# Kernel optimization log

Measured on AMD Instinct MI355X. Metric: run time of the kernel, lower is better.

The kernel has to match this reference:

```python
import jax, jax.numpy as jnp
import numpy as np
from jax import lax

K = 3  # AdaConv kernel_size inside conv_block


def conv2d(x, w, b, pad):
    # x: (B,C,H,W), w: (O,I,kh,kw) -> NCHW conv with symmetric padding
    y = lax.conv_general_dilated(x, w, (1, 1), [(pad, pad), (pad, pad)],
                                 dimension_numbers=('NCHW', 'OIHW', 'NCHW'))
    return y + b[None, :, None, None]


def unfold3(x):
    # nn.Unfold(kernel=3, pad=1): patches ordered channel-major then (kh,kw) row-major
    B, C, H, W = x.shape
    xp = jnp.pad(x, ((0, 0), (0, 0), (1, 1), (1, 1)))
    return jnp.stack([xp[:, :, i:i + H, j:j + W]
                      for i in range(K) for j in range(K)], axis=2)  # (B,C,9,H,W)


def adaconv(x, mask, aw_w, aw_b, mt_w, mt_b, c_w, c_b):
    # groups=1, groups_channels=out_ch in this configuration
    weight = conv2d(mask, aw_w, aw_b, pad=2)          # (B, 9, H, W)
    x = conv2d(x, c_w, c_b, pad=1)                    # (B, out_ch, H, W)
    p = unfold3(x)                                    # (B, out_ch, 9, H, W)
    out = jnp.einsum('bkhw,bckhw->bchw', weight, p)   # per-pixel adaptive conv
    mask2 = conv2d(mask, mt_w, mt_b, pad=2)
    return out, mask2


def lrelu(x):
    return jax.nn.leaky_relu(x, 0.01)


def setup_inputs() -> dict:
    key = jax.random.key(0)
    ks = jax.random.split(key, 20)
    B, Cin, Cout, Mi, Mo, H, W = 2, 64, 64, 64, 64, 256, 256
    s = 0.05
    d = {
        'x': jax.random.normal(ks[0], (B, Cin, H, W), jnp.float32),
        'mask': jax.random.normal(ks[1], (B, Mi, H, W), jnp.float32),
        # AdaConv 1 (in_ch->out_ch, mask_in->mask_out)
        'aw1_w': jax.random.normal(ks[2], (K * K, Mi, 2 * K - 1, 2 * K - 1), jnp.float32) * s,
        'aw1_b': jax.random.normal(ks[3], (K * K,), jnp.float32) * s,
        'mt1_w': jax.random.normal(ks[4], (Mo, Mi, 2 * K - 1, 2 * K - 1), jnp.float32) * s,
        'mt1_b': jax.random.normal(ks[5], (Mo,), jnp.float32) * s,
        'c1_w': jax.random.normal(ks[6], (Cout, Cin, K, K), jnp.float32) * s,
        'c1_b': jax.random.normal(ks[7], (Cout,), jnp.float32) * s,
        # AdaConv 2 (out_ch->out_ch, mask_out->mask_out)
        'aw2_w': jax.random.normal(ks[8], (K * K, Mo, 2 * K - 1, 2 * K - 1), jnp.float32) * s,
        'aw2_b': jax.random.normal(ks[9], (K * K,), jnp.float32) * s,
        'mt2_w': jax.random.normal(ks[10], (Mo, Mo, 2 * K - 1, 2 * K - 1), jnp.float32) * s,
        'mt2_b': jax.random.normal(ks[11], (Mo,), jnp.float32) * s,
        'c2_w': jax.random.normal(ks[12], (Cout, Cout, K, K), jnp.float32) * s,
        'c2_b': jax.random.normal(ks[13], (Cout,), jnp.float32) * s,
        # 1x1 residual conv
        'cr_w': jax.random.normal(ks[14], (Cout, Cin, 1, 1), jnp.float32) * s,
        'cr_b': jax.random.normal(ks[15], (Cout,), jnp.float32) * s,
    }
    return d


def reference(x, mask, aw1_w, aw1_b, mt1_w, mt1_b, c1_w, c1_b,
              aw2_w, aw2_b, mt2_w, mt2_b, c2_w, c2_b, cr_w, cr_b):
    res = conv2d(x, cr_w, cr_b, pad=0)
    x, mask = adaconv(x, mask, aw1_w, aw1_b, mt1_w, mt1_b, c1_w, c1_b)
    x, mask = lrelu(x), lrelu(mask)
    x, mask = adaconv(x, mask, aw2_w, aw2_b, mt2_w, mt2_b, c2_w, c2_b)
    x, mask = lrelu(x), lrelu(mask)
    return (x + res, mask)
```

## Files before the change

kernel.cpp:

```cpp
#include <hip/hip_runtime.h>

#define HWSZ 65536
#define CCH  64

typedef __bf16 bf16x8 __attribute__((ext_vector_type(8)));
typedef __bf16 bf16x4 __attribute__((ext_vector_type(4)));
typedef float  f32x4  __attribute__((ext_vector_type(4)));

__device__ inline void gload_lds16(const void* g, void* l) {
    __builtin_amdgcn_global_load_lds(
        (const __attribute__((address_space(1))) void*)g,
        (__attribute__((address_space(3))) void*)l, 16, 0, 0);
}

__global__ __launch_bounds__(256) void k_cvt(
    const float* __restrict__ src, __bf16* __restrict__ dst)
{
    int p  = blockIdx.x * 256 + threadIdx.x;
    int b  = p >> 16, hw = p & 65535;
    const float* sp = src + (((size_t)b * 64) << 16) + hw;
    __bf16* dp = dst + (size_t)p * 64;
    #pragma unroll
    for (int c8 = 0; c8 < 8; ++c8) {
        bf16x8 v8;
        #pragma unroll
        for (int j = 0; j < 8; ++j)
            v8[j] = (__bf16)sp[(size_t)(c8 * 8 + j) << 16];
        *(bf16x8*)(dp + c8 * 8) = v8;
    }
}

__global__ __launch_bounds__(256) void k_prep3(
    const float* __restrict__ src, __bf16* __restrict__ dst)
{
    int t = blockIdx.x * 256 + threadIdx.x;
    if (t >= 9 * 64 * 64) return;
    int j = t & 7;
    int u = (t >> 3) % 512;
    int k = t / 4096;
    int o = u >> 3;
    int s = (u & 7) ^ (o & 7);
    int i = s * 8 + j;
    dst[t] = (__bf16)src[((size_t)o * 64 + i) * 9 + k];
}

__global__ __launch_bounds__(256) void k_prepF(
    const float* __restrict__ mt, const float* __restrict__ aw,
    __bf16* __restrict__ dst)
{
    int t = blockIdx.x * 256 + threadIdx.x;
    if (t >= 25 * 96 * 64) return;
    int j = t & 7;
    int u = (t >> 3) % 768;
    int k = t / 6144;
    int r = u >> 3;
    int s = (u & 7) ^ (r & 7);
    int i = s * 8 + j;
    float v = 0.f;
    if (r < 64)      v = mt[((size_t)r * 64 + i) * 25 + k];
    else if (r < 73) v = aw[((size_t)(r - 64) * 64 + i) * 25 + k];
    dst[t] = (__bf16)v;
}

template<int KSZ, int MFT, int RELU, int EPI>
__global__ __launch_bounds__(256) void k_mconv(
    const __bf16* __restrict__ xh, const __bf16* __restrict__ wb,
    const float* __restrict__ bias, const float* __restrict__ bias2,
    float* __restrict__ outf, __bf16* __restrict__ outh,
    float* __restrict__ out2)
{
    constexpr int PAD   = KSZ / 2;
    constexpr int TW    = 16 + 2 * PAD;
    constexpr int NPIX  = TW * TW;
    constexpr int KK    = KSZ * KSZ;
    constexpr int SROWS = (MFT == 5) ? 96 : 64;
    constexpr int SLICE = SROWS * 128;
    constexpr int NISS  = SROWS / 32;

    __shared__ __align__(16) __bf16 lx[NPIX * 64];
    __shared__ __align__(16) __bf16 lw[2][SROWS * 64];
    __shared__ float lb[80];

    const int t    = threadIdx.x;
    const int w0   = blockIdx.x * 16, h0 = blockIdx.y * 16, b = blockIdx.z;
    const int wvv  = t >> 6;
    const int lane = t & 63;
    const int px   = lane & 15;
    const int g    = lane >> 4;

    auto STAGE = [&](int k, int buf) {
        const char* gs = (const char*)wb + (size_t)k * SLICE;
        char* lbase = (char*)lw[buf];
        #pragma unroll
        for (int r = 0; r < NISS; ++r) {
            int ub = (wvv * NISS + r) * 64;
            gload_lds16(gs + (ub + lane) * 16, lbase + ub * 16);
        }
    };

    STAGE(0, 0);
    STAGE(1, 1);

    if (t < 64) lb[t] = bias[t];
    if constexpr (MFT == 5) {
        if (t >= 64 && t < 80) lb[t] = (t - 64 < 9) ? bias2[t - 64] : 0.f;
    }

    bf16x8 zv;
    #pragma unroll
    for (int j = 0; j < 8; ++j) zv[j] = (__bf16)0.f;
    constexpr int PITER = (NPIX + 255) / 256;
    #pragma unroll
    for (int pi = 0; pi < PITER; ++pi) {
        int pix = pi * 256 + t;
        if (pix < NPIX) {
            int sy = pix / TW, sx = pix - sy * TW;
            int gy = h0 + sy - PAD, gx = w0 + sx - PAD;
            bool ok = (unsigned)gy < 256u && (unsigned)gx < 256u;
            const __bf16* src = xh + ((((size_t)b << 16) + gy * 256 + gx) << 6);
            int rowbase = pix << 7, sw = (pix & 7) << 4;
            #pragma unroll
            for (int c8 = 0; c8 < 8; ++c8) {
                bf16x8 v8 = ok ? *(const bf16x8*)(src + c8 * 8) : zv;
                *(bf16x8*)((char*)lx + rowbase + ((c8 << 4) ^ sw)) = v8;
            }
        }
    }
    __syncthreads();

    f32x4 acc[MFT][4];
    #pragma unroll
    for (int m = 0; m < MFT; ++m)
        #pragma unroll
        for (int nf = 0; nf < 4; ++nf)
            acc[m][nf] = (f32x4){0.f, 0.f, 0.f, 0.f};

    #pragma unroll
    for (int k = 0; k < KK; ++k) {
        const __bf16* lwb = lw[k & 1];
        const int dy = k / KSZ, dx = k - dy * KSZ;

        bf16x8 bfr[4][2];
        #pragma unroll
        for (int nf = 0; nf < 4; ++nf) {
            int pix = (wvv * 4 + nf + dy) * TW + (px + dx);
            int rowbase = pix << 7, sw = (pix & 7) << 4;
            #pragma unroll
            for (int ks = 0; ks < 2; ++ks)
                bfr[nf][ks] = *(const bf16x8*)((const char*)lx + rowbase + ((((ks * 4 + g) << 4)) ^ sw));
        }
        bf16x8 afr[MFT][2];
        #pragma unroll
        for (int m = 0; m < MFT; ++m) {
            int o = m * 16 + px;
            int rowbase = o << 7, sw = (o & 7) << 4;
            #pragma unroll
            for (int ks = 0; ks < 2; ++ks)
                afr[m][ks] = *(const bf16x8*)((const char*)lwb + rowbase + ((((ks * 4 + g) << 4)) ^ sw));
        }
        #pragma unroll
        for (int m = 0; m < MFT; ++m)
            #pragma unroll
            for (int nf = 0; nf < 4; ++nf)
                #pragma unroll
                for (int ks = 0; ks < 2; ++ks)
                    acc[m][nf] = __builtin_amdgcn_mfma_f32_16x16x32_bf16(
                        afr[m][ks], bfr[nf][ks], acc[m][nf], 0, 0, 0);

        if (k == KK - 1) break;

        asm volatile("s_waitcnt lgkmcnt(0)" ::: "memory");
        __builtin_amdgcn_sched_barrier(0);
        __builtin_amdgcn_s_barrier();
        bool issued = (k + 2 < KK);
        if (issued) {
            STAGE(k + 2, k & 1);
            if constexpr (NISS == 2) asm volatile("s_waitcnt vmcnt(2)" ::: "memory");
            else                     asm volatile("s_waitcnt vmcnt(3)" ::: "memory");
        } else {
            asm volatile("s_waitcnt vmcnt(0)" ::: "memory");
        }
        __builtin_amdgcn_sched_barrier(0);
        __builtin_amdgcn_s_barrier();
    }

    #pragma unroll
    for (int m = 0; m < MFT; ++m) {
        #pragma unroll
        for (int nf = 0; nf < 4; ++nf) {
            int row = h0 + wvv * 4 + nf, col = w0 + px;
            if (m < 4) {
                float vj[4];
                #pragma unroll
                for (int j = 0; j < 4; ++j) {
                    float v = acc[m][nf][j] + lb[m * 16 + g * 4 + j];
                    if (RELU) v = v > 0.f ? v : 0.01f * v;
                    vj[j] = v;
                }
                if constexpr (EPI == 0) {
                    bf16x4 pk;
                    #pragma unroll
                    for (int j = 0; j < 4; ++j) pk[j] = (__bf16)vj[j];
                    *(bf16x4*)(outh + ((((size_t)b << 16) + row * 256 + col) << 6)
                                    + m * 16 + g * 4) = pk;
                } else {
                    #pragma unroll
                    for (int j = 0; j < 4; ++j)
                        outf[((size_t)(b * 64 + m * 16 + g * 4 + j) << 16)
                             + row * 256 + col] = vj[j];
                }
            } else {
                #pragma unroll
                for (int j = 0; j < 4; ++j) {
                    int o2 = g * 4 + j;
                    if (o2 < 9)
                        out2[((size_t)(b * 9 + o2) << 16) + row * 256 + col]
                            = acc[m][nf][j] + lb[64 + o2];
                }
            }
        }
    }
}

__global__ __launch_bounds__(256) void k_conv1x1(
    const __bf16* __restrict__ xh, const float* __restrict__ w,
    const float* __restrict__ bias, float* __restrict__ out)
{
    __shared__ __align__(16) float lwT[4096];
    __shared__ float lb[64];
    int t = threadIdx.x;
    for (int s = t; s < 4096; s += 256) lwT[s] = w[(s & 63) * 64 + (s >> 6)];
    if (t < 64) lb[t] = bias[t];
    __syncthreads();

    int p  = blockIdx.x * 256 + t;
    int b  = p >> 16, hw = p & 65535;
    const __bf16* xp = xh + (size_t)p * 64;

    float acc[64];
    #pragma unroll
    for (int o = 0; o < 64; ++o) acc[o] = lb[o];

    #pragma unroll
    for (int c8 = 0; c8 < 8; ++c8) {
        bf16x8 v8 = *(const bf16x8*)(xp + c8 * 8);
        #pragma unroll
        for (int j = 0; j < 8; ++j) {
            float xi = (float)v8[j];
            const float4* w4 = (const float4*)&lwT[(c8 * 8 + j) * 64];
            #pragma unroll
            for (int o4 = 0; o4 < 16; ++o4) {
                float4 wv = w4[o4];
                acc[o4*4+0] += wv.x * xi;
                acc[o4*4+1] += wv.y * xi;
                acc[o4*4+2] += wv.z * xi;
                acc[o4*4+3] += wv.w * xi;
            }
        }
    }
    float* op = out + (((size_t)b * 64) << 16) + hw;
    #pragma unroll
    for (int o = 0; o < 64; ++o) op[(size_t)o << 16] = acc[o];
}

__global__ __launch_bounds__(256, 4) void k_ada1(
    const float* __restrict__ wgt, const __bf16* __restrict__ xin,
    __bf16* __restrict__ outh)
{
    int t  = threadIdx.x;
    int pg = t >> 3, c8 = t & 7;
    int p  = blockIdx.x * 32 + pg;
    int b  = p >> 16, hw = p & 65535;
    int h  = hw >> 8, wc = hw & 255;

    const float* wp = wgt + ((size_t)(b * 9) << 16) + hw;
    const __bf16* cen = xin + (size_t)p * 64 + c8 * 8;

    float wk[9];
    const __bf16* nbp[9];
    #pragma unroll
    for (int dy = 0; dy < 3; ++dy)
        #pragma unroll
        for (int dx = 0; dx < 3; ++dx) {
            int k = dy * 3 + dx;
            bool ok = ((unsigned)(h + dy - 1) < 256u) &&
                      ((unsigned)(wc + dx - 1) < 256u);
            wk[k]  = ok ? wp[(size_t)k << 16] : 0.f;
            nbp[k] = ok ? cen + ((dy - 1) * 256 + (dx - 1)) * 64 : cen;
        }

    float acc[8] = {0.f,0.f,0.f,0.f,0.f,0.f,0.f,0.f};
    #pragma unroll
    for (int k = 0; k < 9; ++k) {
        bf16x8 v8 = *(const bf16x8*)nbp[k];
        float w = wk[k];
        #pragma unroll
        for (int j = 0; j < 8; ++j) acc[j] += w * (float)v8[j];
    }

    bf16x8 o8;
    #pragma unroll
    for (int j = 0; j < 8; ++j) {
        float v = acc[j];
        o8[j] = (__bf16)(v > 0.f ? v : 0.01f * v);
    }
    *(bf16x8*)(outh + (size_t)p * 64 + c8 * 8) = o8;
}

__global__ __launch_bounds__(256, 4) void k_ada2(
    const float* __restrict__ wgt, const __bf16* __restrict__ x2h,
    float* __restrict__ outf)
{
    __shared__ float ls[32 * 65];

    int t  = threadIdx.x;
    int pg = t >> 3, c8 = t & 7;
    int p  = blockIdx.x * 32 + pg;
    int b  = p >> 16, hw = p & 65535;
    int h  = hw >> 8, wc = hw & 255;

    const float* wp = wgt + ((size_t)(b * 9) << 16) + hw;
    const __bf16* cen = x2h + (size_t)p * 64 + c8 * 8;

    float wk[9];
    const __bf16* nbp[9];
    #pragma unroll
    for (int dy = 0; dy < 3; ++dy)
        #pragma unroll
        for (int dx = 0; dx < 3; ++dx) {
            int k = dy * 3 + dx;
            bool ok = ((unsigned)(h + dy - 1) < 256u) &&
                      ((unsigned)(wc + dx - 1) < 256u);
            wk[k]  = ok ? wp[(size_t)k << 16] : 0.f;
            nbp[k] = ok ? cen + ((dy - 1) * 256 + (dx - 1)) * 64 : cen;
        }

    float acc[8] = {0.f,0.f,0.f,0.f,0.f,0.f,0.f,0.f};
    #pragma unroll
    for (int k = 0; k < 9; ++k) {
        bf16x8 v8 = *(const bf16x8*)nbp[k];
        float w = wk[k];
        #pragma unroll
        for (int j = 0; j < 8; ++j) acc[j] += w * (float)v8[j];
    }

    #pragma unroll
    for (int j = 0; j < 8; ++j) {
        float v = acc[j];
        ls[pg * 65 + c8 * 8 + j] = v > 0.f ? v : 0.01f * v;
    }
    __syncthreads();

    int pbase = blockIdx.x * 32;
    int bb    = pbase >> 16, hwb = pbase & 65535;
    int pix   = t & 31, cq = t >> 5;
    #pragma unroll
    for (int i = 0; i < 8; ++i) {
        int c = i * 8 + cq;
        float v = ls[pix * 65 + c];
        float* op = outf + ((size_t)(bb * 64 + c) << 16) + hwb + pix;
        *op = *op + v;
    }
}

extern "C" void kernel_launch(void* const* d_in, const int* in_sizes, int n_in,
                              void* d_out, int out_size, void* d_ws, size_t ws_size,
                              hipStream_t stream)
{
    const float* x     = (const float*)d_in[0];
    const float* mask  = (const float*)d_in[1];
    const float* aw1_w = (const float*)d_in[2];
    const float* aw1_b = (const float*)d_in[3];
    const float* mt1_w = (const float*)d_in[4];
    const float* mt1_b = (const float*)d_in[5];
    const float* c1_w  = (const float*)d_in[6];
    const float* c1_b  = (const float*)d_in[7];
    const float* aw2_w = (const float*)d_in[8];
    const float* aw2_b = (const float*)d_in[9];
    const float* mt2_w = (const float*)d_in[10];
    const float* mt2_b = (const float*)d_in[11];
    const float* c2_w  = (const float*)d_in[12];
    const float* c2_b  = (const float*)d_in[13];
    const float* cr_w  = (const float*)d_in[14];
    const float* cr_b  = (const float*)d_in[15];

    float* out_x = (float*)d_out;
    float* out_m = (float*)d_out + 8388608;

    float*  wgt  = (float*)d_ws;
    __bf16* xh   = (__bf16*)((char*)d_ws + 4718592);
    __bf16* mh   = (__bf16*)((char*)d_ws + 21495808);
    __bf16* x2h  = mh;
    __bf16* wbase = (__bf16*)((char*)d_ws + 38273024);
    __bf16* wb_c1 = wbase;
    __bf16* wb_c2 = wbase + 36864;
    __bf16* wb_F1 = wbase + 73728;
    __bf16* wb_F2 = wbase + 227328;

    __bf16* maska_h = (__bf16*)out_x;
    __bf16* xa_h    = (__bf16*)out_x + 8388608;
    __bf16* x1_h    = (__bf16*)out_m;

    dim3 blk(256);
    dim3 gconv(16, 16, 2);
    dim3 gpix(512);
    dim3 gada(4096);

    k_cvt<<<gpix, blk, 0, stream>>>(x,    xh);
    k_cvt<<<gpix, blk, 0, stream>>>(mask, mh);
    k_prep3<<<144, blk, 0, stream>>>(c1_w, wb_c1);
    k_prep3<<<144, blk, 0, stream>>>(c2_w, wb_c2);
    k_prepF<<<600, blk, 0, stream>>>(mt1_w, aw1_w, wb_F1);
    k_prepF<<<600, blk, 0, stream>>>(mt2_w, aw2_w, wb_F2);

    k_mconv<5,5,1,0><<<gconv, blk, 0, stream>>>(mh, wb_F1, mt1_b, aw1_b,
                                                nullptr, maska_h, wgt);
    k_mconv<3,4,0,0><<<gconv, blk, 0, stream>>>(xh, wb_c1, c1_b, nullptr,
                                                nullptr, x1_h, nullptr);
    k_ada1<<<gada, blk, 0, stream>>>(wgt, x1_h, xa_h);
    k_mconv<5,5,1,1><<<gconv, blk, 0, stream>>>(maska_h, wb_F2, mt2_b, aw2_b,
                                                out_m, nullptr, wgt);
    k_mconv<3,4,0,0><<<gconv, blk, 0, stream>>>(xa_h, wb_c2, c2_b, nullptr,
                                                nullptr, x2h, nullptr);
    k_conv1x1<<<gpix, blk, 0, stream>>>(xh, cr_w, cr_b, out_x);
    k_ada2<<<gada, blk, 0, stream>>>(wgt, x2h, out_x);
}
```

Measured before the change: 205.6 us.

## Merge launches into horizontal super-kernels and split conv K-dim into two halves

Replaces the six prep launches with one block-dispatched prep kernel. The mask/x convolutions of each stage now run as a single horizontally fused launch, with the 1x1 residual conv folded into the second. The conv body now loads input channels in two 32-channel halves, which cuts LDS per block (no swizzle) so four blocks can fit per CU under launch_bounds(256,4). The costs are a second staging pass with an extra barrier, possible LDS bank conflicts from dropping the XOR swizzle, and intermediate buffers moved into workspace.

```diff
diff --git a/kernel.cpp b/kernel.cpp
--- a/kernel.cpp
+++ b/kernel.cpp
@@ -13,10 +13,11 @@
         (__attribute__((address_space(3))) void*)l, 16, 0, 0);
 }
 
-__global__ __launch_bounds__(256) void k_cvt(
-    const float* __restrict__ src, __bf16* __restrict__ dst)
-{
-    int p  = blockIdx.x * 256 + threadIdx.x;
+
+__device__ void cvt_body(int cb, const float* __restrict__ src,
+                         __bf16* __restrict__ dst)
+{
+    int p  = cb * 256 + threadIdx.x;
     int b  = p >> 16, hw = p & 65535;
     const float* sp = src + (((size_t)b * 64) << 16) + hw;
     __bf16* dp = dst + (size_t)p * 64;
@@ -30,32 +31,26 @@
     }
 }
 
-__global__ __launch_bounds__(256) void k_prep3(
-    const float* __restrict__ src, __bf16* __restrict__ dst)
-{
-    int t = blockIdx.x * 256 + threadIdx.x;
-    if (t >= 9 * 64 * 64) return;
-    int j = t & 7;
-    int u = (t >> 3) % 512;
-    int k = t / 4096;
-    int o = u >> 3;
-    int s = (u & 7) ^ (o & 7);
-    int i = s * 8 + j;
-    dst[t] = (__bf16)src[((size_t)o * 64 + i) * 9 + k];
-}
-
-__global__ __launch_bounds__(256) void k_prepF(
-    const float* __restrict__ mt, const float* __restrict__ aw,
-    __bf16* __restrict__ dst)
-{
-    int t = blockIdx.x * 256 + threadIdx.x;
-    if (t >= 25 * 96 * 64) return;
-    int j = t & 7;
-    int u = (t >> 3) % 768;
-    int k = t / 6144;
-    int r = u >> 3;
-    int s = (u & 7) ^ (r & 7);
-    int i = s * 8 + j;
+__device__ void prep3_body(int cb, const float* __restrict__ src,
+                           __bf16* __restrict__ dst)
+{
+    int t = cb * 256 + threadIdx.x;
+    int ii = t & 31;
+    int o  = (t >> 5) & 63;
+    int r  = t >> 11;
+    int k  = r % 9, ci = r / 9;
+    dst[t] = (__bf16)src[((size_t)o * 64 + ci * 32 + ii) * 9 + k];
+}
+
+__device__ void prepF_body(int cb, const float* __restrict__ mt,
+                           const float* __restrict__ aw, __bf16* __restrict__ dst)
+{
+    int t = cb * 256 + threadIdx.x;
+    int ii = t & 31;
+    int r  = (t >> 5) % 96;
+    int q  = t / 3072;
+    int k  = q % 25, ci = q / 25;
+    int i  = ci * 32 + ii;
     float v = 0.f;
     if (r < 64)      v = mt[((size_t)r * 64 + i) * 25 + k];
     else if (r < 73) v = aw[((size_t)(r - 64) * 64 + i) * 25 + k];
@@ -63,7 +58,7 @@
 }
 
 template<int KSZ, int MFT, int RELU, int EPI>
-__global__ __launch_bounds__(256) void k_mconv(
+__device__ void mconv_body(char* smem, int bx, int by, int b,
     const __bf16* __restrict__ xh, const __bf16* __restrict__ wb,
     const float* __restrict__ bias, const float* __restrict__ bias2,
     float* __restrict__ outf, __bf16* __restrict__ outh,
@@ -74,114 +69,105 @@
     constexpr int NPIX  = TW * TW;
     constexpr int KK    = KSZ * KSZ;
     constexpr int SROWS = (MFT == 5) ? 96 : 64;
-    constexpr int SLICE = SROWS * 128;
-    constexpr int NISS  = SROWS / 32;
-
-    __shared__ __align__(16) __bf16 lx[NPIX * 64];
-    __shared__ __align__(16) __bf16 lw[2][SROWS * 64];
-    __shared__ float lb[80];
+    constexpr int SLICE = SROWS * 64;
+
+    __bf16* lx  = (__bf16*)smem;
+    __bf16* lw0 = lx + NPIX * 32;
+    __bf16* lw1 = lw0 + SROWS * 32;
+    float*  lb  = (float*)(lw1 + SROWS * 32);
 
     const int t    = threadIdx.x;
-    const int w0   = blockIdx.x * 16, h0 = blockIdx.y * 16, b = blockIdx.z;
+    const int w0   = bx * 16, h0 = by * 16;
     const int wvv  = t >> 6;
     const int lane = t & 63;
     const int px   = lane & 15;
     const int g    = lane >> 4;
 
-    auto STAGE = [&](int k, int buf) {
-        const char* gs = (const char*)wb + (size_t)k * SLICE;
-        char* lbase = (char*)lw[buf];
-        #pragma unroll
-        for (int r = 0; r < NISS; ++r) {
-            int ub = (wvv * NISS + r) * 64;
-            gload_lds16(gs + (ub + lane) * 16, lbase + ub * 16);
+    auto STAGE = [&](int ci, int k, __bf16* lbuf) {
+        const char* gs = (const char*)wb + (size_t)(ci * KK + k) * SLICE;
+        if constexpr (MFT == 5) {
+            if (wvv < 3) {
+                #pragma unroll
+                for (int r = 0; r < 2; ++r) {
+                    int ub = wvv * 128 + r * 64;
+                    gload_lds16(gs + (ub + lane) * 16, (char*)lbuf + ub * 16);
+                }
+            }
+        } else {
+            int ub = wvv * 64;
+            gload_lds16(gs + (ub + lane) * 16, (char*)lbuf + ub * 16);
         }
     };
-
-    STAGE(0, 0);
-    STAGE(1, 1);
 
     if (t < 64) lb[t] = bias[t];
     if constexpr (MFT == 5) {
         if (t >= 64 && t < 80) lb[t] = (t - 64 < 9) ? bias2[t - 64] : 0.f;
     }
 
-    bf16x8 zv;
-    #pragma unroll
-    for (int j = 0; j < 8; ++j) zv[j] = (__bf16)0.f;
-    constexpr int PITER = (NPIX + 255) / 256;
-    #pragma unroll
-    for (int pi = 0; pi < PITER; ++pi) {
-        int pix = pi * 256 + t;
-        if (pix < NPIX) {
+    f32x4 acc[MFT][4];
+    #pragma unroll
+    for (int m = 0; m < MFT; ++m)
+        #pragma unroll
+        for (int nf = 0; nf < 4; ++nf)
+            acc[m][nf] = (f32x4){0.f, 0.f, 0.f, 0.f};
+
+    for (int ci = 0; ci < 2; ++ci) {
+        if (ci) __syncthreads();
+        STAGE(ci, 0, lw0);
+        STAGE(ci, 1, lw1);
+
+        bf16x8 zv;
+        #pragma unroll
+        for (int j = 0; j < 8; ++j) zv[j] = (__bf16)0.f;
+        for (int e = t; e < NPIX * 4; e += 256) {
+            int pix = e >> 2, c4 = e & 3;
             int sy = pix / TW, sx = pix - sy * TW;
             int gy = h0 + sy - PAD, gx = w0 + sx - PAD;
             bool ok = (unsigned)gy < 256u && (unsigned)gx < 256u;
-            const __bf16* src = xh + ((((size_t)b << 16) + gy * 256 + gx) << 6);
-            int rowbase = pix << 7, sw = (pix & 7) << 4;
+            bf16x8 v8 = zv;
+            if (ok) v8 = *(const bf16x8*)(xh + ((((size_t)b << 16) + gy * 256 + gx) << 6)
+                                          + ci * 32 + c4 * 8);
+            *(bf16x8*)(lx + pix * 32 + c4 * 8) = v8;
+        }
+        __syncthreads();
+
+        #pragma unroll
+        for (int k = 0; k < KK; ++k) {
+            __bf16* lwb = (k & 1) ? lw1 : lw0;
+            const int dy = k / KSZ, dx = k - dy * KSZ;
+
+            bf16x8 bfr[4];
             #pragma unroll
-            for (int c8 = 0; c8 < 8; ++c8) {
-                bf16x8 v8 = ok ? *(const bf16x8*)(src + c8 * 8) : zv;
-                *(bf16x8*)((char*)lx + rowbase + ((c8 << 4) ^ sw)) = v8;
-            }
-        }
-    }
-    __syncthreads();
-
-    f32x4 acc[MFT][4];
-    #pragma unroll
-    for (int m = 0; m < MFT; ++m)
-        #pragma unroll
-        for (int nf = 0; nf < 4; ++nf)
-            acc[m][nf] = (f32x4){0.f, 0.f, 0.f, 0.f};
-
-    #pragma unroll
-    for (int k = 0; k < KK; ++k) {
-        const __bf16* lwb = lw[k & 1];
-        const int dy = k / KSZ, dx = k - dy * KSZ;
-
-        bf16x8 bfr[4][2];
-        #pragma unroll
-        for (int nf = 0; nf < 4; ++nf) {
-            int pix = (wvv * 4 + nf + dy) * TW + (px + dx);
-            int rowbase = pix << 7, sw = (pix & 7) << 4;
+            for (int nf = 0; nf < 4; ++nf) {
+                int pix = (wvv * 4 + nf + dy) * TW + (px + dx);
+                bfr[nf] = *(const bf16x8*)(lx + pix * 32 + g * 8);
+            }
             #pragma unroll
-            for (int ks = 0; ks < 2; ++ks)
-                bfr[nf][ks] = *(const bf16x8*)((const char*)lx + rowbase + ((((ks * 4 + g) << 4)) ^ sw));
-        }
-        bf16x8 afr[MFT][2];
-        #pragma unroll
-        for (int m = 0; m < MFT; ++m) {
-            int o = m * 16 + px;
-            int rowbase = o << 7, sw = (o & 7) << 4;
-            #pragma unroll
-            for (int ks = 0; ks < 2; ++ks)
-                afr[m][ks] = *(const bf16x8*)((const char*)lwb + rowbase + ((((ks * 4 + g) << 4)) ^ sw));
-        }
-        #pragma unroll
-        for (int m = 0; m < MFT; ++m)
-            #pragma unroll
-            for (int nf = 0; nf < 4; ++nf)
+            for (int m = 0; m < MFT; ++m) {
+                bf16x8 afr = *(const bf16x8*)(lwb + (m * 16 + px) * 32 + g * 8);
                 #pragma unroll
-                for (int ks = 0; ks < 2; ++ks)
+                for (int nf = 0; nf < 4; ++nf)
                     acc[m][nf] = __builtin_amdgcn_mfma_f32_16x16x32_bf16(
-                        afr[m][ks], bfr[nf][ks], acc[m][nf], 0, 0, 0);
-
-        if (k == KK - 1) break;
-
-        asm volatile("s_waitcnt lgkmcnt(0)" ::: "memory");
-        __builtin_amdgcn_sched_barrier(0);
-        __builtin_amdgcn_s_barrier();
-        bool issued = (k + 2 < KK);
-        if (issued) {
-            STAGE(k + 2, k & 1);
-            if constexpr (NISS == 2) asm volatile("s_waitcnt vmcnt(2)" ::: "memory");
-            else                     asm volatile("s_waitcnt vmcnt(3)" ::: "memory");
-        } else {
-            asm volatile("s_waitcnt vmcnt(0)" ::: "memory");
-        }
-        __builtin_amdgcn_sched_barrier(0);
-        __builtin_amdgcn_s_barrier();
+                        afr, bfr[nf], acc[m][nf], 0, 0, 0);
+            }
+
+            if (k == KK - 1) break;
+
+            asm volatile("s_waitcnt lgkmcnt(0)" ::: "memory");
+            __builtin_amdgcn_sched_barrier(0);
+            __builtin_amdgcn_s_barrier();
+            bool issued = (k + 2 < KK);
+            if (issued) STAGE(ci, k + 2, (k & 1) ? lw1 : lw0);
+            if constexpr (MFT == 5) {
+                if (issued && wvv < 3) asm volatile("s_waitcnt vmcnt(2)" ::: "memory");
+                else                   asm volatile("s_waitcnt vmcnt(0)" ::: "memory");
+            } else {
+                if (issued) asm volatile("s_waitcnt vmcnt(1)" ::: "memory");
+                else        asm volatile("s_waitcnt vmcnt(0)" ::: "memory");
+            }
+            __builtin_amdgcn_sched_barrier(0);
+            __builtin_amdgcn_s_barrier();
+        }
     }
 
     #pragma unroll
@@ -222,18 +208,18 @@
     }
 }
 
-__global__ __launch_bounds__(256) void k_conv1x1(
+__device__ void conv1x1_body(char* smem, int cb,
     const __bf16* __restrict__ xh, const float* __restrict__ w,
     const float* __restrict__ bias, float* __restrict__ out)
 {
-    __shared__ __align__(16) float lwT[4096];
-    __shared__ float lb[64];
+    float* lwT = (float*)smem;
+    float* lb  = lwT + 4096;
     int t = threadIdx.x;
     for (int s = t; s < 4096; s += 256) lwT[s] = w[(s & 63) * 64 + (s >> 6)];
     if (t < 64) lb[t] = bias[t];
     __syncthreads();
 
-    int p  = blockIdx.x * 256 + t;
+    int p  = cb * 256 + t;
     int b  = p >> 16, hw = p & 65535;
     const __bf16* xp = xh + (size_t)p * 64;
 
@@ -261,6 +247,63 @@
     float* op = out + (((size_t)b * 64) << 16) + hw;
     #pragma unroll
     for (int o = 0; o < 64; ++o) op[(size_t)o << 16] = acc[o];
+}
+
+
+__global__ __launch_bounds__(256) void k_prep(
+    const float* x, const float* mask,
+    const float* c1w, const float* c2w,
+    const float* mt1w, const float* aw1w,
+    const float* mt2w, const float* aw2w,
+    __bf16* xh, __bf16* mh,
+    __bf16* wbc1, __bf16* wbc2, __bf16* wbF1, __bf16* wbF2)
+{
+    int bid = blockIdx.x;
+    if      (bid < 512)  cvt_body(bid, x, xh);
+    else if (bid < 1024) cvt_body(bid - 512, mask, mh);
+    else if (bid < 1168) prep3_body(bid - 1024, c1w, wbc1);
+    else if (bid < 1312) prep3_body(bid - 1168, c2w, wbc2);
+    else if (bid < 1912) prepF_body(bid - 1312, mt1w, aw1w, wbF1);
+    else                 prepF_body(bid - 1912, mt2w, aw2w, wbF2);
+}
+
+__global__ __launch_bounds__(256, 4) void k_super1(
+    const __bf16* mh, const __bf16* xh,
+    const __bf16* wbF1, const __bf16* wbc1,
+    const float* mt1_b, const float* aw1_b, const float* c1_b,
+    __bf16* maska, float* wgt, __bf16* x1h)
+{
+    __shared__ __align__(16) char smem[38400];
+    int bid = blockIdx.x;
+    if (bid < 512) {
+        mconv_body<5,5,1,0>(smem, bid & 15, (bid >> 4) & 15, bid >> 8,
+                            mh, wbF1, mt1_b, aw1_b, nullptr, maska, wgt);
+    } else {
+        int r = bid - 512;
+        mconv_body<3,4,0,0>(smem, r & 15, (r >> 4) & 15, r >> 8,
+                            xh, wbc1, c1_b, nullptr, nullptr, x1h, nullptr);
+    }
+}
+
+__global__ __launch_bounds__(256, 4) void k_super2(
+    const __bf16* maska, const __bf16* xah, const __bf16* xh,
+    const __bf16* wbF2, const __bf16* wbc2,
+    const float* mt2_b, const float* aw2_b, const float* c2_b,
+    const float* crw, const float* crb,
+    float* outm, float* wgt, __bf16* x2h, float* outx)
+{
+    __shared__ __align__(16) char smem[38400];
+    int bid = blockIdx.x;
+    if (bid < 512) {
+        mconv_body<5,5,1,1>(smem, bid & 15, (bid >> 4) & 15, bid >> 8,
+                            maska, wbF2, mt2_b, aw2_b, outm, nullptr, wgt);
+    } else if (bid < 1024) {
+        int r = bid - 512;
+        mconv_body<3,4,0,0>(smem, r & 15, (r >> 4) & 15, r >> 8,
+                            xah, wbc2, c2_b, nullptr, nullptr, x2h, nullptr);
+    } else {
+        conv1x1_body(smem, bid - 1024, xh, crw, crb, outx);
+    }
 }
 
 __global__ __launch_bounds__(256, 4) void k_ada1(
@@ -387,41 +430,31 @@
     float* out_x = (float*)d_out;
     float* out_m = (float*)d_out + 8388608;
 
-    float*  wgt  = (float*)d_ws;
-    __bf16* xh   = (__bf16*)((char*)d_ws + 4718592);
-    __bf16* mh   = (__bf16*)((char*)d_ws + 21495808);
-    __bf16* x2h  = mh;
+    float*  wgt   = (float*)d_ws;
+    __bf16* xh    = (__bf16*)((char*)d_ws + 4718592);
+    __bf16* mh    = (__bf16*)((char*)d_ws + 21495808);
+    __bf16* x2h   = mh;
     __bf16* wbase = (__bf16*)((char*)d_ws + 38273024);
     __bf16* wb_c1 = wbase;
     __bf16* wb_c2 = wbase + 36864;
     __bf16* wb_F1 = wbase + 73728;
     __bf16* wb_F2 = wbase + 227328;
-
-    __bf16* maska_h = (__bf16*)out_x;
-    __bf16* xa_h    = (__bf16*)out_x + 8388608;
-    __bf16* x1_h    = (__bf16*)out_m;
+    __bf16* maska = (__bf16*)((char*)d_ws + 39034880);
+    __bf16* xah   = (__bf16*)((char*)d_ws + 55812096);
+    __bf16* x1h   = (__bf16*)out_m;
 
     dim3 blk(256);
-    dim3 gconv(16, 16, 2);
-    dim3 gpix(512);
-    dim3 gada(4096);
-
-    k_cvt<<<gpix, blk, 0, stream>>>(x,    xh);
-    k_cvt<<<gpix, blk, 0, stream>>>(mask, mh);
-    k_prep3<<<144, blk, 0, stream>>>(c1_w, wb_c1);
-    k_prep3<<<144, blk, 0, stream>>>(c2_w, wb_c2);
-    k_prepF<<<600, blk, 0, stream>>>(mt1_w, aw1_w, wb_F1);
-    k_prepF<<<600, blk, 0, stream>>>(mt2_w, aw2_w, wb_F2);
-
-    k_mconv<5,5,1,0><<<gconv, blk, 0, stream>>>(mh, wb_F1, mt1_b, aw1_b,
-                                                nullptr, maska_h, wgt);
-    k_mconv<3,4,0,0><<<gconv, blk, 0, stream>>>(xh, wb_c1, c1_b, nullptr,
-                                                nullptr, x1_h, nullptr);
-    k_ada1<<<gada, blk, 0, stream>>>(wgt, x1_h, xa_h);
-    k_mconv<5,5,1,1><<<gconv, blk, 0, stream>>>(maska_h, wb_F2, mt2_b, aw2_b,
-                                                out_m, nullptr, wgt);
-    k_mconv<3,4,0,0><<<gconv, blk, 0, stream>>>(xa_h, wb_c2, c2_b, nullptr,
-                                                nullptr, x2h, nullptr);
-    k_conv1x1<<<gpix, blk, 0, stream>>>(xh, cr_w, cr_b, out_x);
-    k_ada2<<<gada, blk, 0, stream>>>(wgt, x2h, out_x);
-}
+
+    k_prep<<<dim3(2512), blk, 0, stream>>>(x, mask, c1_w, c2_w,
+        mt1_w, aw1_w, mt2_w, aw2_w, xh, mh, wb_c1, wb_c2, wb_F1, wb_F2);
+
+    k_super1<<<dim3(1024), blk, 0, stream>>>(mh, xh, wb_F1, wb_c1,
+        mt1_b, aw1_b, c1_b, maska, wgt, x1h);
+
+    k_ada1<<<dim3(4096), blk, 0, stream>>>(wgt, x1h, xah);
+
+    k_super2<<<dim3(1536), blk, 0, stream>>>(maska, xah, xh, wb_F2, wb_c2,
+        mt2_b, aw2_b, c2_b, cr_w, cr_b, out_m, wgt, x2h, out_x);
+
+    k_ada2<<<dim3(4096), blk, 0, stream>>>(wgt, x2h, out_x);
+}
```

New measurement: 258.1 us. +25.6%, slower.
